# Optimization experiments

Measured on AMD Instinct MI355X. Metric: run time of the kernel, lower is better.

The kernel has to match this reference:

```python
import jax, jax.numpy as jnp
import numpy as np

B, E, D = 16, 42, 256  # batch, entity grid side, feature dim


def setup_inputs() -> dict:
    key = jax.random.key(0)
    k1, k2, k3, k4, k5 = jax.random.split(key, 5)
    inp = jax.random.normal(k1, (B, E, E, D), dtype=jnp.float32)
    mem = jax.random.normal(k2, (B, E, E, D), dtype=jnp.float32)
    mask = jax.random.randint(k3, (B, E, E), 0, 2) > 0  # bool, True = keep
    w_lin = jax.random.normal(k4, (1, D), dtype=jnp.float32) * (1.0 / np.sqrt(D))
    dot_scale = jax.random.uniform(k5, (D,), dtype=jnp.float32,
                                   minval=0.0, maxval=1.0 / np.sqrt(D))
    return {"input": inp, "memory": mem, "mask": mask,
            "w_lin": w_lin, "dot_scale": dot_scale}


def reference(input, memory, mask, w_lin, dot_scale):
    b, e, _, d = input.shape
    n = e * e
    x = input.reshape(b, n, d)
    m = memory.reshape(b, n, d)
    msk = mask.reshape(b, n)
    # additive term: per-query scalar from linear projection  [b, n, 1]
    input_dot = x @ w_lin.T
    # scaled dot-product scores  [b, n, n]
    cross_dot = jnp.einsum('bnd,bmd->bnm', x * dot_scale, m)
    att = input_dot + cross_dot
    # mask: subtract huge constant where mask is False (torch: -1e30 * ~mask)
    att = att - 1e30 * (~msk)[:, None, :].astype(att.dtype)
    weight_one = jax.nn.softmax(att, axis=-1)
    output_one = jnp.einsum('bnm,bmd->bnd', weight_one, m)
    out = jnp.concatenate([x, output_one], axis=-1)
    return out.reshape(b, e, e, 2 * d)
```

## Files before the change

kernel.cpp:

```cpp
#include <hip/hip_runtime.h>

#define NQ 1764
#define NQP 1792
#define DIM 256
#define KT 32
#define NT 56
#define QBLK 64

#define RM_SZ (KT * DIM)
#define TR_SZ (DIM * KT)
#define BUF_SZ (RM_SZ + TR_SZ)
#define P_OFF (2 * BUF_SZ)
#define P_STRIDE 40
#define SM_TOTAL (P_OFF + 4 * 16 * P_STRIDE)

#define WS_MRM_SZ (16 * NQP * DIM)
#define WS_MTR_SZ (16 * DIM * NQP)

typedef __attribute__((ext_vector_type(4))) short short4v;
typedef __attribute__((ext_vector_type(8))) short short8v;
typedef __attribute__((ext_vector_type(4))) float float4v;

static __device__ __forceinline__ ushort f2bf(float f) {
  union { float f; unsigned u; } v; v.f = f;
  return (ushort)((v.u + 0x7FFFu + ((v.u >> 16) & 1u)) >> 16);
}

static __device__ __forceinline__ void dma16(const void* g, void* l) {
  __builtin_amdgcn_global_load_lds(
      (__attribute__((address_space(1))) void*)(void*)g,
      (__attribute__((address_space(3))) void*)l, 16, 0, 0);
}

__global__ __launch_bounds__(256)
void prep_m(const float* __restrict__ mg, ushort* __restrict__ mrm,
            ushort* __restrict__ mtr)
{
  __shared__ float smf[64 * 260];
  const int tid = threadIdx.x;
  const int b   = blockIdx.x & 15;
  const int kt  = blockIdx.x >> 4;
  const int k0  = kt * 64;
  const float* mb = mg + (size_t)b * NQ * DIM;

  #pragma unroll
  for (int i = 0; i < 16; ++i) {
    const int idx = i * 256 + tid;
    const int row = idx >> 6;
    const int ch  = idx & 63;
    const int c4  = ch * 4;
    const int gk  = k0 + row;
    float4v v = (gk < NQ) ? *(const float4v*)(mb + (size_t)gk * DIM + c4)
                          : (float4v){0.f, 0.f, 0.f, 0.f};
    *(float4v*)&smf[row * 260 + ((ch ^ (row >> 3)) << 2)] = v;
    union { short4v v4; short e[4]; } h;
    #pragma unroll
    for (int j = 0; j < 4; ++j) h.e[j] = (short)f2bf(v[j]);
    *(short4v*)(mrm + ((size_t)b * NQP + k0 + row) * DIM + c4) = h.v4;
  }
  __syncthreads();

  const int wv = tid >> 6;
  const int ln = tid & 63;
  const int dr = ln >> 3;
  const int kc = ln & 7;
  #pragma unroll
  for (int it = 0; it < 8; ++it) {
    const int d  = wv * 64 + it * 8 + dr;
    const int dc = d >> 2;
    const int de = d & 3;
    union { short8v v; short e[8]; } u;
    #pragma unroll
    for (int j = 0; j < 8; ++j)
      u.e[j] = (short)f2bf(smf[(kc * 8 + j) * 260 + ((dc ^ kc) << 2) + de]);
    *(short8v*)(mtr + ((size_t)b * DIM + d) * NQP + k0 + kc * 8) = u.v;
  }
}


static __device__ __forceinline__ void stage_tile(const ushort* mrb, const ushort* mtb,
                                                  ushort* smb, int k0, int w, int lane)
{
  #pragma unroll
  for (int j = 0; j < 4; ++j) {
    const int L  = (w * 4 + j) * 64 + lane;
    const int k  = L >> 5;
    const int cs = L & 31;
    const int gc = cs ^ (k & 7);
    dma16(mrb + (size_t)(k0 + k) * DIM + gc * 8, smb + (w * 4 + j) * 512);
  }
  #pragma unroll
  for (int j = 0; j < 4; ++j) {
    const int L = (w * 4 + j) * 64 + lane;
    const int d = L >> 2;
    const int t = L & 3;
    const int kc = (t ^ (d & 3) ^ ((d >> 2) & 3)) & 3;
    dma16(mtb + (size_t)d * NQP + k0 + kc * 8, smb + RM_SZ + (w * 4 + j) * 512);
  }
}

__global__ __launch_bounds__(256, 2)
void attn_fused(const float* __restrict__ x, const ushort* __restrict__ mrm,
                const ushort* __restrict__ mtr, const int* __restrict__ maskg,
                const float* __restrict__ scale, float* __restrict__ out)
{
  __shared__ ushort sm[SM_TOTAL];
  const int tid  = threadIdx.x;
  const int w    = tid >> 6;
  const int lane = tid & 63;
  const int l15  = lane & 15;
  const int quad = lane >> 4;
  const int l7   = l15 & 7;

  const int b      = blockIdx.x & 15;
  const int qblk   = blockIdx.x >> 4;
  const int qbase0 = qblk * QBLK;
  const int qbase  = qbase0 + w * 16;

  const float*  xb  = x + (size_t)b * NQ * DIM;
  const ushort* mrb = mrm + (size_t)b * NQP * DIM;
  const ushort* mtb = mtr + (size_t)b * DIM * NQP;
  const int*    mkb = maskg + (size_t)b * NQ;
  float*        ob  = out + (size_t)b * NQ * (2 * DIM);

  short8v qa[8];
  {
    int q0 = qbase + l15; q0 = q0 < NQ ? q0 : NQ - 1;
    const float* xr0 = xb + (size_t)q0 * DIM;
    #pragma unroll
    for (int kk = 0; kk < 8; ++kk) {
      const int dof = kk * 32 + quad * 8;
      const float4v sa = *(const float4v*)(scale + dof);
      const float4v sb = *(const float4v*)(scale + dof + 4);
      const float4v a0 = *(const float4v*)(xr0 + dof);
      const float4v a1 = *(const float4v*)(xr0 + dof + 4);
      union { short8v v; short e[8]; } u0;
      #pragma unroll
      for (int j = 0; j < 4; ++j) {
        u0.e[j]     = (short)f2bf(a0[j] * sa[j]);
        u0.e[j + 4] = (short)f2bf(a1[j] * sb[j]);
      }
      qa[kk] = u0.v;
    }
  }

  float4v o[16];
  #pragma unroll
  for (int dt = 0; dt < 16; ++dt) o[dt] = (float4v){0.f, 0.f, 0.f, 0.f};
  float l0[4] = {0.f, 0.f, 0.f, 0.f};

  stage_tile(mrb, mtb, sm, 0, w, lane);
  int mvc[2];
  #pragma unroll
  for (int ks = 0; ks < 2; ++ks) {
    const int key = ks * 16 + l15;
    mvc[ks] = (key < NQ) ? mkb[key] : 0;
  }

  #pragma unroll 1
  for (int t = 0; t < NT; ++t) {
    __syncthreads();
    if (t + 1 < NT)
      stage_tile(mrb, mtb, sm + ((t + 1) & 1) * BUF_SZ, (t + 1) * KT, w, lane);

    int mvn[2] = {0, 0};
    if (t + 1 < NT) {
      #pragma unroll
      for (int ks = 0; ks < 2; ++ks) {
        const int key = (t + 1) * KT + ks * 16 + l15;
        mvn[ks] = (key < NQ) ? mkb[key] : 0;
      }
    }

    const ushort* rmp = sm + (t & 1) * BUF_SZ;
    const ushort* trp = rmp + RM_SZ;

    #pragma unroll
    for (int ks = 0; ks < 2; ++ks) {
      float4v sA = (float4v){0.f, 0.f, 0.f, 0.f};
      float4v sB = (float4v){0.f, 0.f, 0.f, 0.f};
      const ushort* rowp = rmp + (ks * 16 + l15) * DIM;
      #pragma unroll
      for (int kk = 0; kk < 4; ++kk) {
        const short8v bvA = *(const short8v*)(rowp + (((kk * 4 + quad) ^ l7) * 8));
        const short8v bvB = *(const short8v*)(rowp + ((((kk + 4) * 4 + quad) ^ l7) * 8));
        sA = __builtin_amdgcn_mfma_f32_16x16x32_bf16(qa[kk], bvA, sA, 0, 0, 0);
        sB = __builtin_amdgcn_mfma_f32_16x16x32_bf16(qa[kk + 4], bvB, sB, 0, 0, 0);
      }
      const int pwc = (((ks * 2 + (l15 >> 3)) ^ quad) << 3) + l7;
      #pragma unroll
      for (int r = 0; r < 4; ++r) {
        const float s = sA[r] + sB[r];
        const float p = mvc[ks] ? exp2f(s * 1.44269504089f) : 0.0f;
        l0[r] += p;
        sm[P_OFF + (w * 16 + quad * 4 + r) * P_STRIDE + pwc] = f2bf(p);
      }
    }
    mvc[0] = mvn[0];
    mvc[1] = mvn[1];

    {
      const int pswz = ((quad ^ (l15 >> 2)) & 3) << 3;
      const short8v pa = *(const short8v*)&sm[P_OFF + (w * 16 + l15) * P_STRIDE + pswz];
      #pragma unroll
      for (int dt = 0; dt < 16; ++dt) {
        const int d = dt * 16 + l15;
        const short8v bv = *(const short8v*)(
            trp + d * KT + (((quad ^ (d & 3) ^ ((d >> 2) & 3)) & 3) * 8));
        o[dt] = __builtin_amdgcn_mfma_f32_16x16x32_bf16(pa, bv, o[dt], 0, 0, 0);
      }
    }
  }

  float il[4];
  #pragma unroll
  for (int r = 0; r < 4; ++r) {
    float a = l0[r];
    a += __shfl_xor(a, 1); a += __shfl_xor(a, 2);
    a += __shfl_xor(a, 4); a += __shfl_xor(a, 8);
    il[r] = 1.0f / a;
  }

  __syncthreads();
  float* fsm = (float*)sm;
  float* ew = fsm + w * 4160;
  #pragma unroll
  for (int dt = 0; dt < 16; ++dt)
    #pragma unroll
    for (int r = 0; r < 4; ++r)
      ew[(quad * 4 + r) * 260 + dt * 16 + l15] = o[dt][r] * il[r];
  #pragma unroll
  for (int i = 0; i < 4; ++i)
    #pragma unroll
    for (int jj = 0; jj < 4; ++jj) {
      const int row = i * 4 + quad;
      const int q   = qbase0 + w * 16 + row;
      if (q < NQ) {
        const float4v v = *(const float4v*)&ew[row * 260 + (jj * 16 + l15) * 4];
        *(float4v*)(ob + (size_t)q * (2 * DIM) + DIM + (jj * 16 + l15) * 4) = v;
      }
    }

  #pragma unroll
  for (int i = 0; i < 16; ++i) {
    const int idx = i * 256 + tid;
    const int row = idx >> 6;
    const int c4  = (idx & 63) * 4;
    const int q   = qbase0 + row;
    if (q < NQ) {
      const float4v v = *(const float4v*)(xb + (size_t)q * DIM + c4);
      *(float4v*)(ob + (size_t)q * (2 * DIM) + c4) = v;
    }
  }
}

extern "C" void kernel_launch(void* const* d_in, const int* in_sizes, int n_in,
                              void* d_out, int out_size, void* d_ws, size_t ws_size,
                              hipStream_t stream) {
  const float* x     = (const float*)d_in[0];
  const float* mem   = (const float*)d_in[1];
  const int*   mask  = (const int*)d_in[2];
  const float* scale = (const float*)d_in[4];
  float* out = (float*)d_out;

  ushort* wsm = (ushort*)d_ws;
  ushort* wst = wsm + WS_MRM_SZ;

  prep_m<<<dim3(448), dim3(256), 0, stream>>>(mem, wsm, wst);
  attn_fused<<<dim3(448), dim3(256), 0, stream>>>(x, wsm, wst, mask, scale, out);
}
```

Measured before the change: 211.7 us.

## Split waves into pairs sharing 32 queries, each wave covering half the keys and output dims

Waves are regrouped into pairs. Each pair owns 32 query rows. For QK^T, each wave of the pair computes scores for half of the 32-key tile across both 16-row query halves. For PV, each wave handles half of the 256 output columns. The aim is more reuse of each LDS B-operand load across two MFMAs, while keeping the register budget similar. In exchange it adds a second __syncthreads per key tile, delays prefetch of the next tile until after the P write, and needs a cross-wave reduction of the softmax denominators through LDS.

```diff
diff --git a/kernel.cpp b/kernel.cpp
--- a/kernel.cpp
+++ b/kernel.cpp
@@ -12,7 +12,9 @@
 #define BUF_SZ (RM_SZ + TR_SZ)
 #define P_OFF (2 * BUF_SZ)
 #define P_STRIDE 40
-#define SM_TOTAL (P_OFF + 4 * 16 * P_STRIDE)
+#define P_SZ (2 * 32 * P_STRIDE)
+#define L_OFF_HW (P_OFF + P_SZ)
+#define SM_TOTAL (L_OFF_HW + 256)
 
 #define WS_MRM_SZ (16 * NQP * DIM)
 #define WS_MTR_SZ (16 * DIM * NQP)
@@ -111,11 +113,13 @@
   const int l15  = lane & 15;
   const int quad = lane >> 4;
   const int l7   = l15 & 7;
+  const int p    = w >> 1;
+  const int h    = w & 1;
 
   const int b      = blockIdx.x & 15;
   const int qblk   = blockIdx.x >> 4;
   const int qbase0 = qblk * QBLK;
-  const int qbase  = qbase0 + w * 16;
+  const int qbase  = qbase0 + p * 32;
 
   const float*  xb  = x + (size_t)b * NQ * DIM;
   const ushort* mrb = mrm + (size_t)b * NQP * DIM;
@@ -123,10 +127,12 @@
   const int*    mkb = maskg + (size_t)b * NQ;
   float*        ob  = out + (size_t)b * NQ * (2 * DIM);
 
-  short8v qa[8];
+  short8v qa0[8], qa1[8];
   {
-    int q0 = qbase + l15; q0 = q0 < NQ ? q0 : NQ - 1;
+    int q0 = qbase + l15;      q0 = q0 < NQ ? q0 : NQ - 1;
+    int q1 = qbase + 16 + l15; q1 = q1 < NQ ? q1 : NQ - 1;
     const float* xr0 = xb + (size_t)q0 * DIM;
+    const float* xr1 = xb + (size_t)q1 * DIM;
     #pragma unroll
     for (int kk = 0; kk < 8; ++kk) {
       const int dof = kk * 32 + quad * 8;
@@ -134,112 +140,144 @@
       const float4v sb = *(const float4v*)(scale + dof + 4);
       const float4v a0 = *(const float4v*)(xr0 + dof);
       const float4v a1 = *(const float4v*)(xr0 + dof + 4);
-      union { short8v v; short e[8]; } u0;
+      const float4v b0 = *(const float4v*)(xr1 + dof);
+      const float4v b1 = *(const float4v*)(xr1 + dof + 4);
+      union { short8v v; short e[8]; } u0, u1;
       #pragma unroll
       for (int j = 0; j < 4; ++j) {
         u0.e[j]     = (short)f2bf(a0[j] * sa[j]);
         u0.e[j + 4] = (short)f2bf(a1[j] * sb[j]);
+        u1.e[j]     = (short)f2bf(b0[j] * sa[j]);
+        u1.e[j + 4] = (short)f2bf(b1[j] * sb[j]);
       }
-      qa[kk] = u0.v;
-    }
-  }
-
-  float4v o[16];
-  #pragma unroll
-  for (int dt = 0; dt < 16; ++dt) o[dt] = (float4v){0.f, 0.f, 0.f, 0.f};
+      qa0[kk] = u0.v;
+      qa1[kk] = u1.v;
+    }
+  }
+
+  float4v o0[8], o1[8];
+  #pragma unroll
+  for (int dt = 0; dt < 8; ++dt) {
+    o0[dt] = (float4v){0.f, 0.f, 0.f, 0.f};
+    o1[dt] = (float4v){0.f, 0.f, 0.f, 0.f};
+  }
   float l0[4] = {0.f, 0.f, 0.f, 0.f};
+  float l1[4] = {0.f, 0.f, 0.f, 0.f};
 
   stage_tile(mrb, mtb, sm, 0, w, lane);
-  int mvc[2];
-  #pragma unroll
-  for (int ks = 0; ks < 2; ++ks) {
-    const int key = ks * 16 + l15;
-    mvc[ks] = (key < NQ) ? mkb[key] : 0;
-  }
+  int mvc = mkb[h * 16 + l15];
+  int mvn = 0;
 
   #pragma unroll 1
   for (int t = 0; t < NT; ++t) {
     __syncthreads();
-    if (t + 1 < NT)
-      stage_tile(mrb, mtb, sm + ((t + 1) & 1) * BUF_SZ, (t + 1) * KT, w, lane);
-
-    int mvn[2] = {0, 0};
-    if (t + 1 < NT) {
-      #pragma unroll
-      for (int ks = 0; ks < 2; ++ks) {
-        const int key = (t + 1) * KT + ks * 16 + l15;
-        mvn[ks] = (key < NQ) ? mkb[key] : 0;
-      }
-    }
 
     const ushort* rmp = sm + (t & 1) * BUF_SZ;
     const ushort* trp = rmp + RM_SZ;
 
-    #pragma unroll
-    for (int ks = 0; ks < 2; ++ks) {
-      float4v sA = (float4v){0.f, 0.f, 0.f, 0.f};
-      float4v sB = (float4v){0.f, 0.f, 0.f, 0.f};
-      const ushort* rowp = rmp + (ks * 16 + l15) * DIM;
+    {
+      float4v s0A = (float4v){0.f, 0.f, 0.f, 0.f};
+      float4v s0B = (float4v){0.f, 0.f, 0.f, 0.f};
+      float4v s1A = (float4v){0.f, 0.f, 0.f, 0.f};
+      float4v s1B = (float4v){0.f, 0.f, 0.f, 0.f};
+      const ushort* rowp = rmp + (h * 16 + l15) * DIM;
       #pragma unroll
       for (int kk = 0; kk < 4; ++kk) {
         const short8v bvA = *(const short8v*)(rowp + (((kk * 4 + quad) ^ l7) * 8));
         const short8v bvB = *(const short8v*)(rowp + ((((kk + 4) * 4 + quad) ^ l7) * 8));
-        sA = __builtin_amdgcn_mfma_f32_16x16x32_bf16(qa[kk], bvA, sA, 0, 0, 0);
-        sB = __builtin_amdgcn_mfma_f32_16x16x32_bf16(qa[kk + 4], bvB, sB, 0, 0, 0);
+        s0A = __builtin_amdgcn_mfma_f32_16x16x32_bf16(qa0[kk], bvA, s0A, 0, 0, 0);
+        s0B = __builtin_amdgcn_mfma_f32_16x16x32_bf16(qa0[kk + 4], bvB, s0B, 0, 0, 0);
+        s1A = __builtin_amdgcn_mfma_f32_16x16x32_bf16(qa1[kk], bvA, s1A, 0, 0, 0);
+        s1B = __builtin_amdgcn_mfma_f32_16x16x32_bf16(qa1[kk + 4], bvB, s1B, 0, 0, 0);
       }
-      const int pwc = (((ks * 2 + (l15 >> 3)) ^ quad) << 3) + l7;
+      const int pwc = (((h * 2 + (l15 >> 3)) ^ quad) << 3) + l7;
       #pragma unroll
       for (int r = 0; r < 4; ++r) {
-        const float s = sA[r] + sB[r];
-        const float p = mvc[ks] ? exp2f(s * 1.44269504089f) : 0.0f;
-        l0[r] += p;
-        sm[P_OFF + (w * 16 + quad * 4 + r) * P_STRIDE + pwc] = f2bf(p);
+        const float pv0 = mvc ? exp2f((s0A[r] + s0B[r]) * 1.44269504089f) : 0.0f;
+        const float pv1 = mvc ? exp2f((s1A[r] + s1B[r]) * 1.44269504089f) : 0.0f;
+        l0[r] += pv0;
+        l1[r] += pv1;
+        sm[P_OFF + (p * 32 + quad * 4 + r) * P_STRIDE + pwc] = f2bf(pv0);
+        sm[P_OFF + (p * 32 + 16 + quad * 4 + r) * P_STRIDE + pwc] = f2bf(pv1);
       }
     }
-    mvc[0] = mvn[0];
-    mvc[1] = mvn[1];
+
+    __syncthreads();
+
+    if (t + 1 < NT) {
+      stage_tile(mrb, mtb, sm + ((t + 1) & 1) * BUF_SZ, (t + 1) * KT, w, lane);
+      const int key = (t + 1) * KT + h * 16 + l15;
+      mvn = (key < NQ) ? mkb[key] : 0;
+    }
 
     {
       const int pswz = ((quad ^ (l15 >> 2)) & 3) << 3;
-      const short8v pa = *(const short8v*)&sm[P_OFF + (w * 16 + l15) * P_STRIDE + pswz];
+      const short8v pa0 = *(const short8v*)&sm[P_OFF + (p * 32 + l15) * P_STRIDE + pswz];
+      const short8v pa1 = *(const short8v*)&sm[P_OFF + (p * 32 + 16 + l15) * P_STRIDE + pswz];
       #pragma unroll
-      for (int dt = 0; dt < 16; ++dt) {
-        const int d = dt * 16 + l15;
+      for (int dt = 0; dt < 8; ++dt) {
+        const int d = (h * 8 + dt) * 16 + l15;
         const short8v bv = *(const short8v*)(
             trp + d * KT + (((quad ^ (d & 3) ^ ((d >> 2) & 3)) & 3) * 8));
-        o[dt] = __builtin_amdgcn_mfma_f32_16x16x32_bf16(pa, bv, o[dt], 0, 0, 0);
+        o0[dt] = __builtin_amdgcn_mfma_f32_16x16x32_bf16(pa0, bv, o0[dt], 0, 0, 0);
+        o1[dt] = __builtin_amdgcn_mfma_f32_16x16x32_bf16(pa1, bv, o1[dt], 0, 0, 0);
       }
     }
-  }
-
-  float il[4];
+    mvc = mvn;
+  }
+
+  float la0[4], la1[4];
   #pragma unroll
   for (int r = 0; r < 4; ++r) {
-    float a = l0[r];
+    float a = l0[r], c = l1[r];
     a += __shfl_xor(a, 1); a += __shfl_xor(a, 2);
     a += __shfl_xor(a, 4); a += __shfl_xor(a, 8);
-    il[r] = 1.0f / a;
-  }
-
+    c += __shfl_xor(c, 1); c += __shfl_xor(c, 2);
+    c += __shfl_xor(c, 4); c += __shfl_xor(c, 8);
+    la0[r] = a;
+    la1[r] = c;
+  }
+
+  float* Lf = (float*)(sm + L_OFF_HW);
+  if (l15 == 0) {
+    #pragma unroll
+    for (int r = 0; r < 4; ++r) {
+      Lf[((p * 2 + 0) * 2 + h) * 16 + quad * 4 + r] = la0[r];
+      Lf[((p * 2 + 1) * 2 + h) * 16 + quad * 4 + r] = la1[r];
+    }
+  }
   __syncthreads();
-  float* fsm = (float*)sm;
-  float* ew = fsm + w * 4160;
-  #pragma unroll
-  for (int dt = 0; dt < 16; ++dt)
-    #pragma unroll
-    for (int r = 0; r < 4; ++r)
-      ew[(quad * 4 + r) * 260 + dt * 16 + l15] = o[dt][r] * il[r];
-  #pragma unroll
-  for (int i = 0; i < 4; ++i)
-    #pragma unroll
-    for (int jj = 0; jj < 4; ++jj) {
-      const int row = i * 4 + quad;
-      const int q   = qbase0 + w * 16 + row;
-      if (q < NQ) {
-        const float4v v = *(const float4v*)&ew[row * 260 + (jj * 16 + l15) * 4];
-        *(float4v*)(ob + (size_t)q * (2 * DIM) + DIM + (jj * 16 + l15) * 4) = v;
-      }
-    }
+  float il0[4], il1[4];
+  #pragma unroll
+  for (int r = 0; r < 4; ++r) {
+    il0[r] = 1.0f / (Lf[((p * 2 + 0) * 2 + 0) * 16 + quad * 4 + r] +
+                     Lf[((p * 2 + 0) * 2 + 1) * 16 + quad * 4 + r]);
+    il1[r] = 1.0f / (Lf[((p * 2 + 1) * 2 + 0) * 16 + quad * 4 + r] +
+                     Lf[((p * 2 + 1) * 2 + 1) * 16 + quad * 4 + r]);
+  }
+
+  float* ew = (float*)sm + p * 8320;
+  #pragma unroll
+  for (int dt = 0; dt < 8; ++dt) {
+    #pragma unroll
+    for (int r = 0; r < 4; ++r) {
+      ew[(quad * 4 + r) * 260 + (h * 8 + dt) * 16 + l15]      = o0[dt][r] * il0[r];
+      ew[(16 + quad * 4 + r) * 260 + (h * 8 + dt) * 16 + l15] = o1[dt][r] * il1[r];
+    }
+  }
+  __syncthreads();
+
+  #pragma unroll
+  for (int i = 0; i < 16; ++i) {
+    const int idx = i * 128 + h * 64 + lane;
+    const int row = idx >> 6;
+    const int c4  = (idx & 63) * 4;
+    const int q   = qbase0 + p * 32 + row;
+    if (q < NQ) {
+      const float4v v = *(const float4v*)&ew[row * 260 + c4];
+      *(float4v*)(ob + (size_t)q * (2 * DIM) + DIM + c4) = v;
+    }
+  }
 
   #pragma unroll
   for (int i = 0; i < 16; ++i) {
```

After: 210.3 us. Within noise of the previous version (-0.7%).
